# Optimization experiments

Measured on AMD Instinct MI355X. Metric: run time of the kernel, lower is better.

## Reference

```python
import jax, jax.numpy as jnp
import numpy as np

T, H, E, I = 1024, 2048, 64, 1024          # tokens, hidden, routed experts, expert ffn dim
N_GROUP, TOPK_GROUP, TOP_K = 8, 4, 8
N_SHARED = 2
ROUTED_SCALE = 2.5
IS = I * N_SHARED                            # shared-expert intermediate size


def setup_inputs() -> dict:
    key = jax.random.key(0)
    ks = jax.random.split(key, 8)
    s = 0.02
    return {
        "hidden_states": jax.random.normal(ks[0], (T, H), jnp.float32),
        "gate_w": jax.random.normal(ks[1], (E, H), jnp.float32) * s,
        "e_bias": jax.random.normal(ks[2], (E,), jnp.float32) * s,
        "w_gate": jax.random.normal(ks[3], (E, I, H), jnp.float32) * s,
        "w_up": jax.random.normal(ks[4], (E, I, H), jnp.float32) * s,
        "w_down": jax.random.normal(ks[5], (E, H, I), jnp.float32) * s,
        "shared_w_gate_up": jax.random.normal(ks[6], (2 * IS, H), jnp.float32) * s,
        "shared_w_down": jax.random.normal(ks[7], (H, IS), jnp.float32) * s,
    }


def _grouped_topk(scores, bias):
    """DeepSeek noaux_tc grouped top-k: sigmoid scores + correction bias,
    pick top `TOPK_GROUP` groups by sum of their top-2 biased scores,
    then top-K experts among allowed groups; weights from unbiased scores."""
    Tn, En = scores.shape
    s = scores + bias[None, :]                                   # [T, E]
    g = s.reshape(Tn, N_GROUP, En // N_GROUP)                    # [T, G, E/G]
    group_scores = jnp.sum(jax.lax.top_k(g, 2)[0], axis=-1)      # [T, G]
    _, gidx = jax.lax.top_k(group_scores, TOPK_GROUP)            # [T, topk_group]
    gmask = jnp.zeros((Tn, N_GROUP), scores.dtype).at[
        jnp.arange(Tn)[:, None], gidx].set(1.0)                  # [T, G]
    smask = jnp.repeat(gmask, En // N_GROUP, axis=1)             # [T, E]
    masked = jnp.where(smask > 0, s, -jnp.inf)
    _, topk_ids = jax.lax.top_k(masked, TOP_K)                   # [T, K]
    w = jnp.take_along_axis(scores, topk_ids, axis=1)            # unbiased scores
    w = w / jnp.sum(w, axis=-1, keepdims=True)                   # renormalize (norm_topk_prob)
    return w, topk_ids


def reference(hidden_states, gate_w, e_bias, w_gate, w_up, w_down,
              shared_w_gate_up, shared_w_down):
    x = hidden_states                                            # [T, H]
    router_logits = x @ gate_w.T                                 # [T, E]
    scores = jax.nn.sigmoid(router_logits)
    topk_w, topk_ids = _grouped_topk(scores, e_bias)             # [T, K] each
    # sparse combine weights [T, E] (zero for unselected experts)
    cw = jnp.zeros((x.shape[0], E), x.dtype).at[
        jnp.arange(x.shape[0])[:, None], topk_ids].add(topk_w)
    # routed experts: dense grouped-GEMM form of the fused-MoE math
    g = jnp.einsum('th,eih->tei', x, w_gate)                     # [T, E, I]
    u = jnp.einsum('th,eih->tei', x, w_up)
    h = jax.nn.silu(g) * u
    routed = jnp.einsum('tei,te,ehi->th', h, cw, w_down)         # [T, H]
    # shared experts MLP (SiluAndMul)
    sg_u = x @ shared_w_gate_up.T                                # [T, 2*IS]
    sg, su = jnp.split(sg_u, 2, axis=-1)
    shared = (jax.nn.silu(sg) * su) @ shared_w_down.T            # [T, H]
    return routed * ROUTED_SCALE + shared
```

## Files before the change

kernel.cpp:

```cpp
#include <hip/hip_runtime.h>
#include <hip/hip_bf16.h>
#include <math.h>

#define T_TOK 1024
#define HID   2048
#define NEXP  64
#define IDIM  1024
#define ISH   2048
#define TOPK  8

typedef float  f32x4  __attribute__((ext_vector_type(4)));
typedef __bf16 bf16x8 __attribute__((ext_vector_type(8)));

#define BM  128
#define BN_ 64
#define BK  64

#define BARRIER_NODRAIN() asm volatile("s_waitcnt lgkmcnt(0)\n\ts_barrier" ::: "memory")

__device__ __forceinline__ bf16x8 cvt8(f32x4 a, f32x4 b) {
  bf16x8 v;
  v[0]=(__bf16)a[0]; v[1]=(__bf16)a[1]; v[2]=(__bf16)a[2]; v[3]=(__bf16)a[3];
  v[4]=(__bf16)b[0]; v[5]=(__bf16)b[1]; v[6]=(__bf16)b[2]; v[7]=(__bf16)b[3];
  return v;
}

__global__ void init_kernel(int* counts) {
  if (threadIdx.x < NEXP) counts[threadIdx.x] = 0;
}

__global__ void xcast_kernel(const float* __restrict__ x, __bf16* __restrict__ xb) {
  long i = ((long)blockIdx.x * 256 + threadIdx.x) * 8;
  f32x4 a = *(const f32x4*)(x + i);
  f32x4 b = *(const f32x4*)(x + i + 4);
  *(bf16x8*)(xb + i) = cvt8(a, b);
}

__global__ __launch_bounds__(256)
void router_kernel(const float* __restrict__ x, const float* __restrict__ gw,
                   const float* __restrict__ eb,
                   int* __restrict__ ids, float* __restrict__ wts,
                   int* __restrict__ counts)
{
  __shared__ __align__(16) float xs[HID];
  __shared__ float red[256];
  __shared__ float sc[NEXP], sb[NEXP];
  const int t = blockIdx.x, tid = threadIdx.x;

  const f32x4* xsrc = (const f32x4*)(x + (long)t * HID);
  f32x4* xd = (f32x4*)xs;
  xd[tid]       = xsrc[tid];
  xd[tid + 256] = xsrc[tid + 256];
  __syncthreads();

  const int e = tid & 63, part = tid >> 6;
  const f32x4* wrow = (const f32x4*)(gw + (long)e * HID + part * 512);
  const f32x4* xrow = (const f32x4*)(xs + part * 512);
  float s = 0.f;
  #pragma unroll 4
  for (int j = 0; j < 128; ++j) {
    f32x4 wv = wrow[j], xv = xrow[j];
    s += wv[0]*xv[0] + wv[1]*xv[1] + wv[2]*xv[2] + wv[3]*xv[3];
  }
  red[tid] = s;
  __syncthreads();
  if (part == 0) {
    float logit = red[e] + red[e+64] + red[e+128] + red[e+192];
    float sig = 1.f / (1.f + expf(-logit));
    sc[e] = sig; sb[e] = sig + eb[e];
  }
  __syncthreads();

  if (tid == 0) {
    float gsc[8];
    for (int g = 0; g < 8; ++g) {
      float m1 = -1e30f, m2 = -1e30f;
      for (int j = 0; j < 8; ++j) {
        float v = sb[g*8 + j];
        if (v > m1) { m2 = m1; m1 = v; } else if (v > m2) m2 = v;
      }
      gsc[g] = m1 + m2;
    }
    unsigned gmask = 0;
    for (int it = 0; it < 4; ++it) {
      int best = 0; float bv = -1e30f;
      for (int g = 0; g < 8; ++g)
        if (!((gmask >> g) & 1) && gsc[g] > bv) { bv = gsc[g]; best = g; }
      gmask |= 1u << best;
    }
    unsigned long long taken = 0;
    int id8[8]; float wsum = 0.f;
    for (int it = 0; it < 8; ++it) {
      int best = 0; float bv = -1e30f;
      for (int e2 = 0; e2 < 64; ++e2) {
        if (!((gmask >> (e2 >> 3)) & 1)) continue;
        if ((taken >> e2) & 1) continue;
        float v = sb[e2];
        if (v > bv) { bv = v; best = e2; }
      }
      taken |= 1ull << best;
      id8[it] = best; wsum += sc[best];
    }
    float inv = 2.5f / wsum;
    for (int k = 0; k < 8; ++k) {
      ids[t*8 + k] = id8[k];
      wts[t*8 + k] = sc[id8[k]] * inv;
      atomicAdd(&counts[id8[k]], 1);
    }
  }
}

__global__ void scan_kernel(const int* __restrict__ counts,
                            int* __restrict__ seg_off, int* __restrict__ cursors,
                            int* __restrict__ pair_e, int* __restrict__ pair_mt,
                            int* __restrict__ npairs) {
  if (threadIdx.x == 0) {
    int off = 0, np = 0;
    for (int e = 0; e < NEXP; ++e) {
      seg_off[e] = off; cursors[e] = off;
      int c = counts[e]; off += c;
      for (int m = 0; m * BM < c; ++m) { pair_e[np] = e; pair_mt[np] = m; ++np; }
    }
    npairs[0] = np;
  }
}

__global__ void scatter_kernel(const int* __restrict__ ids, const float* __restrict__ wts,
                               int* __restrict__ cursors,
                               int* __restrict__ tok_list, float* __restrict__ wgt_list,
                               int* __restrict__ pos_of) {
  int idx = blockIdx.x * 256 + threadIdx.x;
  if (idx >= T_TOK * TOPK) return;
  int t = idx >> 3;
  int e = ids[idx];
  int pos = atomicAdd(&cursors[e], 1);
  tok_list[pos] = t;
  wgt_list[pos] = wts[idx];
  pos_of[idx] = pos;
}

template<int EPI, bool ROUTED, bool GATHER>
__global__ __launch_bounds__(256, 1)
void gemm_dma(const __bf16* __restrict__ A, const float* __restrict__ Bg0,
              const float* __restrict__ Bu0, long strideBe, int ldB, int K,
              void* Cg, void* Cu, int ldc,
              const int* __restrict__ pair_e, const int* __restrict__ pair_mt,
              const int* __restrict__ npairs,
              const int* __restrict__ seg_off, const int* __restrict__ seg_cnt,
              const int* __restrict__ tok_list, int Mfull)
{
  __shared__ __align__(16) char smem[3 * 32768];
  const int tid = threadIdx.x, lane = tid & 63, wv = tid >> 6;

  int e, mt0, soff, cnt;
  if (ROUTED) {
    int p = blockIdx.y;
    if (p >= npairs[0]) return;
    e = pair_e[p]; mt0 = pair_mt[p]; soff = seg_off[e]; cnt = seg_cnt[e];
  } else {
    e = 0; mt0 = blockIdx.y; soff = 0; cnt = Mfull;
  }
  const int rem = cnt - mt0 * BM;
  if (rem <= 0) return;

  const float* B0 = (gridDim.z == 2 && blockIdx.z) ? Bu0 : Bg0;
  void* Cout      = (gridDim.z == 2 && blockIdx.z) ? Cu  : Cg;
  const float* Bb0 = B0 + (long)e * strideBe;

  const __bf16* srcA[4];
  const float*  srcB[4];
  #pragma unroll
  for (int i = 0; i < 4; ++i) {
    int row = wv * 32 + i * 8 + (lane >> 3);
    int kcA = (lane & 7) ^ (row & 7);
    int rr  = (row < rem) ? row : (rem - 1);
    int idx = soff + mt0 * BM + rr;
    long arow = GATHER ? (long)tok_list[idx] : (long)idx;
    srcA[i] = A + arow * (long)K + kcA * 8;

    int col = wv * 16 + i * 4 + (lane >> 4);
    int kcB = (lane & 15) ^ (col & 15);
    srcB[i] = Bb0 + (long)(blockIdx.x * BN_ + col) * ldB + kcB * 4;
  }

#define STAGE(b, kk) { \
  char* Ad = smem + (b) * 32768 + wv * 4096; \
  char* Bd = Ad + 16384; \
  _Pragma("unroll") \
  for (int i = 0; i < 4; ++i) \
    __builtin_amdgcn_global_load_lds((const __attribute__((address_space(1))) void*)(srcA[i] + (kk)), \
        (__attribute__((address_space(3))) void*)(Ad + i * 1024), 16, 0, 0); \
  _Pragma("unroll") \
  for (int i = 0; i < 4; ++i) \
    __builtin_amdgcn_global_load_lds((const __attribute__((address_space(1))) void*)(srcB[i] + (kk)), \
        (__attribute__((address_space(3))) void*)(Bd + i * 1024), 16, 0, 0); }

  f32x4 acc[8] = {};
  const int c15 = lane & 15, hi = lane >> 4;

#define COMPUTE(b) { \
  char* Ab = smem + (b) * 32768; \
  char* Bbuf = Ab + 16384; \
  _Pragma("unroll") \
  for (int kh = 0; kh < 2; ++kh) { \
    const int colL = wv * 16 + c15; \
    const int kc = kh * 8 + hi * 2; \
    f32x4 b0 = *(const f32x4*)(Bbuf + colL * 256 + (((kc    ) ^ c15) << 4)); \
    f32x4 b1 = *(const f32x4*)(Bbuf + colL * 256 + (((kc + 1) ^ c15) << 4)); \
    bf16x8 bfrag = cvt8(b0, b1); \
    const int physA = ((kh * 4 + hi) ^ (lane & 7)) << 4; \
    _Pragma("unroll") \
    for (int m = 0; m < 8; ++m) { \
      bf16x8 af = *(const bf16x8*)(Ab + (m * 16 + c15) * 128 + physA); \
      acc[m] = __builtin_amdgcn_mfma_f32_16x16x32_bf16(af, bfrag, acc[m], 0, 0, 0); \
    } \
  } }

  const int NT = K / BK;
  STAGE(0, 0);
  STAGE(1, BK);
  for (int t = 0; t < NT; ++t) {
    asm volatile("s_waitcnt vmcnt(8)" ::: "memory");
    BARRIER_NODRAIN();
    const int kk = (t + 2 < NT) ? (t + 2) * BK : 0;
    STAGE((t + 2) % 3, kk);
    COMPUTE(t % 3);
  }
#undef STAGE
#undef COMPUTE

  asm volatile("s_waitcnt vmcnt(0)" ::: "memory");
  BARRIER_NODRAIN();

  if (EPI == 0) {
    __bf16* Cs = (__bf16*)smem;
    #pragma unroll
    for (int m = 0; m < 8; ++m) {
      #pragma unroll
      for (int r = 0; r < 4; ++r) {
        int row = m * 16 + hi * 4 + r;
        Cs[row * 64 + wv * 16 + c15] = (__bf16)acc[m][r];
      }
    }
    BARRIER_NODRAIN();
    __bf16* Cb = (__bf16*)Cout;
    #pragma unroll
    for (int p = 0; p < 4; ++p) {
      int row = p * 32 + (tid >> 3);
      if (row < rem)
        *(bf16x8*)(Cb + (long)(soff + mt0 * BM + row) * ldc + blockIdx.x * BN_ + (tid & 7) * 8) =
            *(const bf16x8*)&Cs[row * 64 + (tid & 7) * 8];
    }
  } else {
    float* O = (float*)Cout;
    const int col = blockIdx.x * BN_ + wv * 16 + c15;
    #pragma unroll
    for (int m = 0; m < 8; ++m) {
      #pragma unroll
      for (int r = 0; r < 4; ++r) {
        int row = m * 16 + hi * 4 + r;
        if (row < rem)
          O[(long)(mt0 * BM + row) * ldc + col] = acc[m][r];
      }
    }
  }
}

__global__ void fuse_kernel(__bf16* __restrict__ g, const __bf16* __restrict__ u,
                            const float* __restrict__ wrow, int rshift) {
  long idx = ((long)blockIdx.x * 256 + threadIdx.x) * 8;
  bf16x8 gv = *(bf16x8*)(g + idx);
  bf16x8 uv = *(const bf16x8*)(u + idx);
  float w = wrow ? wrow[idx >> rshift] : 1.f;
  bf16x8 h;
  #pragma unroll
  for (int j = 0; j < 8; ++j) {
    float gf = (float)gv[j], uf = (float)uv[j];
    h[j] = (__bf16)(w * gf * uf / (1.f + __expf(-gf)));
  }
  *(bf16x8*)(g + idx) = h;
}

__global__ __launch_bounds__(256)
void combine_kernel(const __bf16* __restrict__ y, const int* __restrict__ pos_of,
                    float* __restrict__ out) {
  const int t = blockIdx.x;
  const int c0 = threadIdx.x * 8;
  float* orow = out + (long)t * HID + c0;
  f32x4 s0 = *(const f32x4*)orow;
  f32x4 s1 = *(const f32x4*)(orow + 4);
  #pragma unroll
  for (int k = 0; k < TOPK; ++k) {
    int row = pos_of[t * TOPK + k];
    bf16x8 v = *(const bf16x8*)(y + (long)row * HID + c0);
    s0[0] += (float)v[0]; s0[1] += (float)v[1]; s0[2] += (float)v[2]; s0[3] += (float)v[3];
    s1[0] += (float)v[4]; s1[1] += (float)v[5]; s1[2] += (float)v[6]; s1[3] += (float)v[7];
  }
  *(f32x4*)orow = s0;
  *(f32x4*)(orow + 4) = s1;
}

extern "C" void kernel_launch(void* const* d_in, const int* in_sizes, int n_in,
                              void* d_out, int out_size, void* d_ws, size_t ws_size,
                              hipStream_t stream) {
  const float* x      = (const float*)d_in[0];
  const float* gate_w = (const float*)d_in[1];
  const float* e_bias = (const float*)d_in[2];
  const float* w_gate = (const float*)d_in[3];
  const float* w_up   = (const float*)d_in[4];
  const float* w_down = (const float*)d_in[5];
  const float* sw_gu  = (const float*)d_in[6];
  const float* sw_d   = (const float*)d_in[7];
  float* out = (float*)d_out;
  char* ws = (char*)d_ws;

  size_t off = 0;
  __bf16* x_bf = (__bf16*)(ws + off);        off += (size_t)T_TOK * HID * 2;
  int*    ids  = (int*)(ws + off);           off += T_TOK * TOPK * 4;
  float*  wts  = (float*)(ws + off);         off += T_TOK * TOPK * 4;
  int* counts  = (int*)(ws + off);           off += 256;
  int* segoff  = (int*)(ws + off);           off += 256;
  int* cursors = (int*)(ws + off);           off += 256;
  int* pair_e  = (int*)(ws + off);           off += 1024;
  int* pair_mt = (int*)(ws + off);           off += 1024;
  int* npairs  = (int*)(ws + off);           off += 256;
  int* tok_list = (int*)(ws + off);          off += T_TOK * TOPK * 4;
  float* wgt_list = (float*)(ws + off);      off += T_TOK * TOPK * 4;
  int* pos_of  = (int*)(ws + off);           off += T_TOK * TOPK * 4;
  off = (off + 255) & ~(size_t)255;
  __bf16* g_buf  = (__bf16*)(ws + off);      off += (size_t)T_TOK * TOPK * IDIM * 2;
  __bf16* u_buf  = (__bf16*)(ws + off);      off += (size_t)T_TOK * TOPK * IDIM * 2;
  __bf16* gs_buf = (__bf16*)(ws + off);      off += (size_t)T_TOK * ISH * 2;
  __bf16* us_buf = (__bf16*)(ws + off);      off += (size_t)T_TOK * ISH * 2;
  __bf16* y_buf  = (__bf16*)(ws + off);      off += (size_t)T_TOK * TOPK * HID * 2;

  init_kernel<<<1, 64, 0, stream>>>(counts);
  xcast_kernel<<<(T_TOK * HID) / (256 * 8), 256, 0, stream>>>(x, x_bf);
  router_kernel<<<T_TOK, 256, 0, stream>>>(x, gate_w, e_bias, ids, wts, counts);
  scan_kernel<<<1, 64, 0, stream>>>(counts, segoff, cursors, pair_e, pair_mt, npairs);
  scatter_kernel<<<(T_TOK * TOPK + 255) / 256, 256, 0, stream>>>(
      ids, wts, cursors, tok_list, wgt_list, pos_of);

  gemm_dma<0, true, true><<<dim3(IDIM / BN_, 128, 2), 256, 0, stream>>>(
      x_bf, w_gate, w_up, (long)IDIM * HID, HID, HID, g_buf, u_buf, IDIM,
      pair_e, pair_mt, npairs, segoff, counts, tok_list, 0);

  fuse_kernel<<<(T_TOK * TOPK * IDIM) / (256 * 8), 256, 0, stream>>>(g_buf, u_buf, wgt_list, 10);

  gemm_dma<0, false, false><<<dim3(ISH / BN_, T_TOK / BM, 2), 256, 0, stream>>>(
      x_bf, sw_gu, sw_gu + (size_t)ISH * HID, 0, HID, HID, gs_buf, us_buf, ISH,
      nullptr, nullptr, nullptr, nullptr, nullptr, nullptr, T_TOK);
  fuse_kernel<<<(T_TOK * ISH) / (256 * 8), 256, 0, stream>>>(gs_buf, us_buf, nullptr, 11);

  gemm_dma<2, false, false><<<dim3(HID / BN_, T_TOK / BM, 1), 256, 0, stream>>>(
      gs_buf, sw_d, sw_d, 0, ISH, ISH, out, out, HID,
      nullptr, nullptr, nullptr, nullptr, nullptr, nullptr, T_TOK);

  gemm_dma<0, true, false><<<dim3(HID / BN_, 128, 1), 256, 0, stream>>>(
      g_buf, w_down, w_down, (long)HID * IDIM, IDIM, IDIM, y_buf, y_buf, HID,
      pair_e, pair_mt, npairs, segoff, counts, tok_list, 0);

  combine_kernel<<<T_TOK, 256, 0, stream>>>(y_buf, pos_of, out);
}
```

Baseline: 653.4 us.

## Split K across waves in GEMM and reduce partial tiles through LDS

The GEMM kernel changes from splitting the output tile's N columns across waves to an intra-block split-K. Each wave now owns a 32-wide K slice of every 128-deep step and computes the full 128x64 tile using its own double-buffered LDS region. Because no wave reads another wave's staged data, the per-step block barriers go away, and each A fragment is reused across four MFMAs. The cost is four times the accumulator registers (32 f32x4 per wave), 128 KB of LDS, and a final cross-wave reduction through LDS before the store.

```diff
diff --git a/kernel.cpp b/kernel.cpp
--- a/kernel.cpp
+++ b/kernel.cpp
@@ -14,9 +14,6 @@
 
 #define BM  128
 #define BN_ 64
-#define BK  64
-
-#define BARRIER_NODRAIN() asm volatile("s_waitcnt lgkmcnt(0)\n\ts_barrier" ::: "memory")
 
 __device__ __forceinline__ bf16x8 cvt8(f32x4 a, f32x4 b) {
   bf16x8 v;
@@ -141,16 +138,17 @@
 
 template<int EPI, bool ROUTED, bool GATHER>
 __global__ __launch_bounds__(256, 1)
-void gemm_dma(const __bf16* __restrict__ A, const float* __restrict__ Bg0,
-              const float* __restrict__ Bu0, long strideBe, int ldB, int K,
-              void* Cg, void* Cu, int ldc,
-              const int* __restrict__ pair_e, const int* __restrict__ pair_mt,
-              const int* __restrict__ npairs,
-              const int* __restrict__ seg_off, const int* __restrict__ seg_cnt,
-              const int* __restrict__ tok_list, int Mfull)
+void gemm_ks(const __bf16* __restrict__ A, const float* __restrict__ Bg0,
+             const float* __restrict__ Bu0, long strideBe, int ldB, int K,
+             void* Cg, void* Cu, int ldc,
+             const int* __restrict__ pair_e, const int* __restrict__ pair_mt,
+             const int* __restrict__ npairs,
+             const int* __restrict__ seg_off, const int* __restrict__ seg_cnt,
+             const int* __restrict__ tok_list, int Mfull)
 {
-  __shared__ __align__(16) char smem[3 * 32768];
+  __shared__ __align__(16) char smem[4 * 32768];
   const int tid = threadIdx.x, lane = tid & 63, wv = tid >> 6;
+  const int c15 = lane & 15, hi = lane >> 4;
 
   int e, mt0, soff, cnt;
   if (ROUTED) {
@@ -167,100 +165,102 @@
   void* Cout      = (gridDim.z == 2 && blockIdx.z) ? Cu  : Cg;
   const float* Bb0 = B0 + (long)e * strideBe;
 
-  const __bf16* srcA[4];
-  const float*  srcB[4];
-  #pragma unroll
-  for (int i = 0; i < 4; ++i) {
-    int row = wv * 32 + i * 8 + (lane >> 3);
-    int kcA = (lane & 7) ^ (row & 7);
+  char* Wb = smem + wv * 32768;
+
+  const __bf16* srcA[8];
+  const float*  srcB[8];
+  #pragma unroll
+  for (int i = 0; i < 8; ++i) {
+    int row = i * 16 + (lane >> 2);
+    int kcA = (lane & 3) ^ (row & 3);
     int rr  = (row < rem) ? row : (rem - 1);
     int idx = soff + mt0 * BM + rr;
     long arow = GATHER ? (long)tok_list[idx] : (long)idx;
-    srcA[i] = A + arow * (long)K + kcA * 8;
-
-    int col = wv * 16 + i * 4 + (lane >> 4);
-    int kcB = (lane & 15) ^ (col & 15);
-    srcB[i] = Bb0 + (long)(blockIdx.x * BN_ + col) * ldB + kcB * 4;
+    srcA[i] = A + arow * (long)K + wv * 32 + kcA * 8;
+
+    int col = i * 8 + (lane >> 3);
+    int kcB = (lane & 7) ^ (col & 7);
+    srcB[i] = Bb0 + (long)(blockIdx.x * BN_ + col) * ldB + wv * 32 + kcB * 4;
   }
 
 #define STAGE(b, kk) { \
-  char* Ad = smem + (b) * 32768 + wv * 4096; \
-  char* Bd = Ad + 16384; \
+  char* Ad = Wb + (b) * 16384; \
+  char* Bd = Ad + 8192; \
   _Pragma("unroll") \
-  for (int i = 0; i < 4; ++i) \
+  for (int i = 0; i < 8; ++i) \
     __builtin_amdgcn_global_load_lds((const __attribute__((address_space(1))) void*)(srcA[i] + (kk)), \
         (__attribute__((address_space(3))) void*)(Ad + i * 1024), 16, 0, 0); \
   _Pragma("unroll") \
-  for (int i = 0; i < 4; ++i) \
+  for (int i = 0; i < 8; ++i) \
     __builtin_amdgcn_global_load_lds((const __attribute__((address_space(1))) void*)(srcB[i] + (kk)), \
         (__attribute__((address_space(3))) void*)(Bd + i * 1024), 16, 0, 0); }
 
-  f32x4 acc[8] = {};
-  const int c15 = lane & 15, hi = lane >> 4;
+  f32x4 acc[8][4] = {};
 
 #define COMPUTE(b) { \
-  char* Ab = smem + (b) * 32768; \
-  char* Bbuf = Ab + 16384; \
+  const char* Al = Wb + (b) * 16384; \
+  const char* Bl = Al + 8192; \
+  bf16x8 bfrag[4]; \
   _Pragma("unroll") \
-  for (int kh = 0; kh < 2; ++kh) { \
-    const int colL = wv * 16 + c15; \
-    const int kc = kh * 8 + hi * 2; \
-    f32x4 b0 = *(const f32x4*)(Bbuf + colL * 256 + (((kc    ) ^ c15) << 4)); \
-    f32x4 b1 = *(const f32x4*)(Bbuf + colL * 256 + (((kc + 1) ^ c15) << 4)); \
-    bf16x8 bfrag = cvt8(b0, b1); \
-    const int physA = ((kh * 4 + hi) ^ (lane & 7)) << 4; \
+  for (int n = 0; n < 4; ++n) { \
+    int col = n * 16 + c15; \
+    f32x4 b0 = *(const f32x4*)(Bl + col * 128 + (((hi * 2    ) ^ (col & 7)) << 4)); \
+    f32x4 b1 = *(const f32x4*)(Bl + col * 128 + (((hi * 2 + 1) ^ (col & 7)) << 4)); \
+    bfrag[n] = cvt8(b0, b1); \
+  } \
+  _Pragma("unroll") \
+  for (int m = 0; m < 8; ++m) { \
+    int row = m * 16 + c15; \
+    bf16x8 af = *(const bf16x8*)(Al + row * 64 + ((hi ^ (row & 3)) << 4)); \
     _Pragma("unroll") \
-    for (int m = 0; m < 8; ++m) { \
-      bf16x8 af = *(const bf16x8*)(Ab + (m * 16 + c15) * 128 + physA); \
-      acc[m] = __builtin_amdgcn_mfma_f32_16x16x32_bf16(af, bfrag, acc[m], 0, 0, 0); \
-    } \
+    for (int n = 0; n < 4; ++n) \
+      acc[m][n] = __builtin_amdgcn_mfma_f32_16x16x32_bf16(af, bfrag[n], acc[m][n], 0, 0, 0); \
   } }
 
-  const int NT = K / BK;
+  const int S = K / 128;
   STAGE(0, 0);
-  STAGE(1, BK);
-  for (int t = 0; t < NT; ++t) {
-    asm volatile("s_waitcnt vmcnt(8)" ::: "memory");
-    BARRIER_NODRAIN();
-    const int kk = (t + 2 < NT) ? (t + 2) * BK : 0;
-    STAGE((t + 2) % 3, kk);
-    COMPUTE(t % 3);
+  for (int s = 0; s < S; ++s) {
+    if (s + 1 < S) {
+      STAGE((s + 1) & 1, (s + 1) * 128);
+      asm volatile("s_waitcnt vmcnt(16)" ::: "memory");
+    } else {
+      asm volatile("s_waitcnt vmcnt(0)" ::: "memory");
+    }
+    COMPUTE(s & 1);
   }
 #undef STAGE
 #undef COMPUTE
 
-  asm volatile("s_waitcnt vmcnt(0)" ::: "memory");
-  BARRIER_NODRAIN();
-
-  if (EPI == 0) {
-    __bf16* Cs = (__bf16*)smem;
+  float* Pw = (float*)Wb;
+  #pragma unroll
+  for (int m = 0; m < 8; ++m)
     #pragma unroll
-    for (int m = 0; m < 8; ++m) {
+    for (int n = 0; n < 4; ++n)
       #pragma unroll
-      for (int r = 0; r < 4; ++r) {
-        int row = m * 16 + hi * 4 + r;
-        Cs[row * 64 + wv * 16 + c15] = (__bf16)acc[m][r];
-      }
-    }
-    BARRIER_NODRAIN();
-    __bf16* Cb = (__bf16*)Cout;
-    #pragma unroll
-    for (int p = 0; p < 4; ++p) {
-      int row = p * 32 + (tid >> 3);
-      if (row < rem)
-        *(bf16x8*)(Cb + (long)(soff + mt0 * BM + row) * ldc + blockIdx.x * BN_ + (tid & 7) * 8) =
-            *(const bf16x8*)&Cs[row * 64 + (tid & 7) * 8];
-    }
-  } else {
-    float* O = (float*)Cout;
-    const int col = blockIdx.x * BN_ + wv * 16 + c15;
-    #pragma unroll
-    for (int m = 0; m < 8; ++m) {
-      #pragma unroll
-      for (int r = 0; r < 4; ++r) {
-        int row = m * 16 + hi * 4 + r;
-        if (row < rem)
-          O[(long)(mt0 * BM + row) * ldc + col] = acc[m][r];
+      for (int r = 0; r < 4; ++r)
+        Pw[(m * 16 + hi * 4 + r) * 64 + n * 16 + c15] = acc[m][n][r];
+  __syncthreads();
+
+  const f32x4* P0 = (const f32x4*)(smem);
+  const f32x4* P1 = (const f32x4*)(smem + 32768);
+  const f32x4* P2 = (const f32x4*)(smem + 65536);
+  const f32x4* P3 = (const f32x4*)(smem + 98304);
+  #pragma unroll
+  for (int j = 0; j < 4; ++j) {
+    int a = j * 2048 + tid * 8;
+    int q = a >> 2;
+    f32x4 v0 = P0[q]     + P1[q]     + P2[q]     + P3[q];
+    f32x4 v1 = P0[q + 1] + P1[q + 1] + P2[q + 1] + P3[q + 1];
+    int row = a >> 6, col = a & 63;
+    if (row < rem) {
+      if (EPI == 0) {
+        __bf16* Cb = (__bf16*)Cout;
+        *(bf16x8*)(Cb + (long)(soff + mt0 * BM + row) * ldc + blockIdx.x * BN_ + col) = cvt8(v0, v1);
+      } else {
+        float* O = (float*)Cout;
+        float* dst = O + (long)(mt0 * BM + row) * ldc + blockIdx.x * BN_ + col;
+        *(f32x4*)dst = v0;
+        *(f32x4*)(dst + 4) = v1;
       }
     }
   }
@@ -341,22 +341,22 @@
   scatter_kernel<<<(T_TOK * TOPK + 255) / 256, 256, 0, stream>>>(
       ids, wts, cursors, tok_list, wgt_list, pos_of);
 
-  gemm_dma<0, true, true><<<dim3(IDIM / BN_, 128, 2), 256, 0, stream>>>(
+  gemm_ks<0, true, true><<<dim3(IDIM / BN_, 128, 2), 256, 0, stream>>>(
       x_bf, w_gate, w_up, (long)IDIM * HID, HID, HID, g_buf, u_buf, IDIM,
       pair_e, pair_mt, npairs, segoff, counts, tok_list, 0);
 
   fuse_kernel<<<(T_TOK * TOPK * IDIM) / (256 * 8), 256, 0, stream>>>(g_buf, u_buf, wgt_list, 10);
 
-  gemm_dma<0, false, false><<<dim3(ISH / BN_, T_TOK / BM, 2), 256, 0, stream>>>(
+  gemm_ks<0, false, false><<<dim3(ISH / BN_, T_TOK / BM, 2), 256, 0, stream>>>(
       x_bf, sw_gu, sw_gu + (size_t)ISH * HID, 0, HID, HID, gs_buf, us_buf, ISH,
       nullptr, nullptr, nullptr, nullptr, nullptr, nullptr, T_TOK);
   fuse_kernel<<<(T_TOK * ISH) / (256 * 8), 256, 0, stream>>>(gs_buf, us_buf, nullptr, 11);
 
-  gemm_dma<2, false, false><<<dim3(HID / BN_, T_TOK / BM, 1), 256, 0, stream>>>(
+  gemm_ks<2, false, false><<<dim3(HID / BN_, T_TOK / BM, 1), 256, 0, stream>>>(
       gs_buf, sw_d, sw_d, 0, ISH, ISH, out, out, HID,
       nullptr, nullptr, nullptr, nullptr, nullptr, nullptr, T_TOK);
 
-  gemm_dma<0, true, false><<<dim3(HID / BN_, 128, 1), 256, 0, stream>>>(
+  gemm_ks<0, true, false><<<dim3(HID / BN_, 128, 1), 256, 0, stream>>>(
       g_buf, w_down, w_down, (long)HID * IDIM, IDIM, IDIM, y_buf, y_buf, HID,
       pair_e, pair_mt, npairs, segoff, counts, tok_list, 0);
 
```

After: 651.0 us (median of 2 runs). About the same (-0.4%).

## Fuse gate/up GEMMs with SiLU epilogue, shrink BK, remap grid for L2 reuse

Applied to the files above, without the earlier changes.

Gate and up projections now run in one GEMM kernel that stages both weight tiles per K-step, accumulates into two accumulator sets, and applies the routing-weighted SiLU-and-mul in the epilogue. This removes the separate fuse kernels and the extra write and read of the g/u intermediate buffers. BK drops from 64 to 32 and launch bounds allow two blocks per CU to restore latency hiding. A 1D grid with a swizzled mapping groups eight M-tiles per N-tile, aiming to reuse weights in cache. The costs are more accumulator registers and more barriers per unit of K.

```diff
diff --git a/kernel.cpp b/kernel.cpp
--- a/kernel.cpp
+++ b/kernel.cpp
@@ -14,7 +14,7 @@
 
 #define BM  128
 #define BN_ 64
-#define BK  64
+#define BK  32
 
 #define BARRIER_NODRAIN() asm volatile("s_waitcnt lgkmcnt(0)\n\ts_barrier" ::: "memory")
 
@@ -139,88 +139,114 @@
   pos_of[idx] = pos;
 }
 
-template<int EPI, bool ROUTED, bool GATHER>
-__global__ __launch_bounds__(256, 1)
-void gemm_dma(const __bf16* __restrict__ A, const float* __restrict__ Bg0,
-              const float* __restrict__ Bu0, long strideBe, int ldB, int K,
-              void* Cg, void* Cu, int ldc,
-              const int* __restrict__ pair_e, const int* __restrict__ pair_mt,
-              const int* __restrict__ npairs,
-              const int* __restrict__ seg_off, const int* __restrict__ seg_cnt,
-              const int* __restrict__ tok_list, int Mfull)
+template<int NS, int EPI, bool ROUTED, bool GATHER>
+__global__ __launch_bounds__(256, 2)
+void gemm_x(const __bf16* __restrict__ A, const float* __restrict__ Bg0,
+            const float* __restrict__ Bu0, long strideBe, int ldB, int K,
+            void* __restrict__ Cout, int ldc, int NTB,
+            const int* __restrict__ pair_e, const int* __restrict__ pair_mt,
+            const int* __restrict__ npairs,
+            const int* __restrict__ seg_off, const int* __restrict__ seg_cnt,
+            const int* __restrict__ tok_list, const float* __restrict__ wgt_list,
+            int Mfull)
 {
-  __shared__ __align__(16) char smem[3 * 32768];
+  constexpr int BUFSZ = (1 + NS) * 8192;
+  __shared__ __align__(16) char smem[3 * BUFSZ];
+  __shared__ float sWs[BM];
   const int tid = threadIdx.x, lane = tid & 63, wv = tid >> 6;
+  const int c15 = lane & 15, hi = lane >> 4;
+
+  const int wgid = blockIdx.x;
+  const int nt   = (wgid >> 3) % NTB;
+  const int p    = (wgid / (8 * NTB)) * 8 + (wgid & 7);
 
   int e, mt0, soff, cnt;
   if (ROUTED) {
-    int p = blockIdx.y;
     if (p >= npairs[0]) return;
     e = pair_e[p]; mt0 = pair_mt[p]; soff = seg_off[e]; cnt = seg_cnt[e];
   } else {
-    e = 0; mt0 = blockIdx.y; soff = 0; cnt = Mfull;
+    if (p >= Mfull / BM) return;
+    e = 0; mt0 = p; soff = 0; cnt = Mfull;
   }
   const int rem = cnt - mt0 * BM;
   if (rem <= 0) return;
 
-  const float* B0 = (gridDim.z == 2 && blockIdx.z) ? Bu0 : Bg0;
-  void* Cout      = (gridDim.z == 2 && blockIdx.z) ? Cu  : Cg;
-  const float* Bb0 = B0 + (long)e * strideBe;
-
-  const __bf16* srcA[4];
-  const float*  srcB[4];
+  const __bf16* srcA[2];
   #pragma unroll
-  for (int i = 0; i < 4; ++i) {
-    int row = wv * 32 + i * 8 + (lane >> 3);
-    int kcA = (lane & 7) ^ (row & 7);
+  for (int i = 0; i < 2; ++i) {
+    int ia  = wv * 2 + i;
+    int row = ia * 16 + (lane >> 2);
+    int kq  = (lane & 3) ^ (row & 3);
     int rr  = (row < rem) ? row : (rem - 1);
     int idx = soff + mt0 * BM + rr;
     long arow = GATHER ? (long)tok_list[idx] : (long)idx;
-    srcA[i] = A + arow * (long)K + kcA * 8;
-
-    int col = wv * 16 + i * 4 + (lane >> 4);
-    int kcB = (lane & 15) ^ (col & 15);
-    srcB[i] = Bb0 + (long)(blockIdx.x * BN_ + col) * ldB + kcB * 4;
+    srcA[i] = A + arow * (long)K + kq * 8;
+  }
+  const float* srcB0[2];
+  const float* srcB1[2];
+  {
+    const float* Bb0 = Bg0 + (long)e * strideBe;
+    const float* Bb1 = Bu0 + (long)e * strideBe;
+    #pragma unroll
+    for (int i = 0; i < 2; ++i) {
+      int ib  = wv * 2 + i;
+      int col = ib * 8 + (lane >> 3);
+      int kq  = (lane & 7) ^ (col & 7);
+      long boff = (long)(nt * BN_ + col) * ldB + kq * 4;
+      srcB0[i] = Bb0 + boff;
+      srcB1[i] = Bb1 + boff;
+    }
   }
 
 #define STAGE(b, kk) { \
-  char* Ad = smem + (b) * 32768 + wv * 4096; \
-  char* Bd = Ad + 16384; \
+  char* base_ = smem + (b) * BUFSZ; \
   _Pragma("unroll") \
-  for (int i = 0; i < 4; ++i) \
+  for (int i = 0; i < 2; ++i) \
     __builtin_amdgcn_global_load_lds((const __attribute__((address_space(1))) void*)(srcA[i] + (kk)), \
-        (__attribute__((address_space(3))) void*)(Ad + i * 1024), 16, 0, 0); \
+        (__attribute__((address_space(3))) void*)(base_ + (wv * 2 + i) * 1024), 16, 0, 0); \
   _Pragma("unroll") \
-  for (int i = 0; i < 4; ++i) \
-    __builtin_amdgcn_global_load_lds((const __attribute__((address_space(1))) void*)(srcB[i] + (kk)), \
-        (__attribute__((address_space(3))) void*)(Bd + i * 1024), 16, 0, 0); }
-
-  f32x4 acc[8] = {};
-  const int c15 = lane & 15, hi = lane >> 4;
+  for (int i = 0; i < 2; ++i) \
+    __builtin_amdgcn_global_load_lds((const __attribute__((address_space(1))) void*)(srcB0[i] + (kk)), \
+        (__attribute__((address_space(3))) void*)(base_ + 8192 + (wv * 2 + i) * 1024), 16, 0, 0); \
+  if constexpr (NS == 2) { \
+    _Pragma("unroll") \
+    for (int i = 0; i < 2; ++i) \
+      __builtin_amdgcn_global_load_lds((const __attribute__((address_space(1))) void*)(srcB1[i] + (kk)), \
+          (__attribute__((address_space(3))) void*)(base_ + 16384 + (wv * 2 + i) * 1024), 16, 0, 0); \
+  } }
+
+  f32x4 accg[8] = {};
+  f32x4 accu[8] = {};
 
 #define COMPUTE(b) { \
-  char* Ab = smem + (b) * 32768; \
-  char* Bbuf = Ab + 16384; \
+  const char* base_ = smem + (b) * BUFSZ; \
+  const int cb = ((wv * 2 + (c15 >> 3)) << 10) + ((c15 & 7) << 7); \
+  const int cx = c15 & 7; \
+  const char* Bl0 = base_ + 8192; \
+  f32x4 g0 = *(const f32x4*)(Bl0 + cb + ((((hi * 2)    ) ^ cx) << 4)); \
+  f32x4 g1 = *(const f32x4*)(Bl0 + cb + ((((hi * 2) + 1) ^ cx) << 4)); \
+  bf16x8 bg = cvt8(g0, g1); \
+  bf16x8 bu = bg; \
+  if constexpr (NS == 2) { \
+    const char* Bl1 = base_ + 16384; \
+    f32x4 u0 = *(const f32x4*)(Bl1 + cb + ((((hi * 2)    ) ^ cx) << 4)); \
+    f32x4 u1 = *(const f32x4*)(Bl1 + cb + ((((hi * 2) + 1) ^ cx) << 4)); \
+    bu = cvt8(u0, u1); \
+  } \
   _Pragma("unroll") \
-  for (int kh = 0; kh < 2; ++kh) { \
-    const int colL = wv * 16 + c15; \
-    const int kc = kh * 8 + hi * 2; \
-    f32x4 b0 = *(const f32x4*)(Bbuf + colL * 256 + (((kc    ) ^ c15) << 4)); \
-    f32x4 b1 = *(const f32x4*)(Bbuf + colL * 256 + (((kc + 1) ^ c15) << 4)); \
-    bf16x8 bfrag = cvt8(b0, b1); \
-    const int physA = ((kh * 4 + hi) ^ (lane & 7)) << 4; \
-    _Pragma("unroll") \
-    for (int m = 0; m < 8; ++m) { \
-      bf16x8 af = *(const bf16x8*)(Ab + (m * 16 + c15) * 128 + physA); \
-      acc[m] = __builtin_amdgcn_mfma_f32_16x16x32_bf16(af, bfrag, acc[m], 0, 0, 0); \
-    } \
+  for (int m = 0; m < 8; ++m) { \
+    bf16x8 af = *(const bf16x8*)(base_ + (m << 10) + (((c15 << 2) + (hi ^ (c15 & 3))) << 4)); \
+    accg[m] = __builtin_amdgcn_mfma_f32_16x16x32_bf16(af, bg, accg[m], 0, 0, 0); \
+    if constexpr (NS == 2) \
+      accu[m] = __builtin_amdgcn_mfma_f32_16x16x32_bf16(af, bu, accu[m], 0, 0, 0); \
   } }
 
   const int NT = K / BK;
   STAGE(0, 0);
   STAGE(1, BK);
   for (int t = 0; t < NT; ++t) {
-    asm volatile("s_waitcnt vmcnt(8)" ::: "memory");
+    if constexpr (NS == 2) asm volatile("s_waitcnt vmcnt(6)" ::: "memory");
+    else                   asm volatile("s_waitcnt vmcnt(4)" ::: "memory");
     BARRIER_NODRAIN();
     const int kk = (t + 2 < NT) ? (t + 2) * BK : 0;
     STAGE((t + 2) % 3, kk);
@@ -229,56 +255,54 @@
 #undef STAGE
 #undef COMPUTE
 
+  if constexpr (NS == 2) {
+    if (tid < BM) {
+      int rr = (tid < rem) ? tid : (rem - 1);
+      sWs[tid] = ROUTED ? wgt_list[soff + mt0 * BM + rr] : 1.f;
+    }
+  }
   asm volatile("s_waitcnt vmcnt(0)" ::: "memory");
-  BARRIER_NODRAIN();
-
-  if (EPI == 0) {
+  __syncthreads();
+
+  if constexpr (EPI == 0) {
     __bf16* Cs = (__bf16*)smem;
     #pragma unroll
     for (int m = 0; m < 8; ++m) {
       #pragma unroll
       for (int r = 0; r < 4; ++r) {
         int row = m * 16 + hi * 4 + r;
-        Cs[row * 64 + wv * 16 + c15] = (__bf16)acc[m][r];
+        float v;
+        if constexpr (NS == 2) {
+          float g = accg[m][r], u = accu[m][r];
+          v = sWs[row] * g * u / (1.f + __expf(-g));
+        } else {
+          v = accg[m][r];
+        }
+        Cs[row * 64 + wv * 16 + c15] = (__bf16)v;
       }
     }
-    BARRIER_NODRAIN();
+    __syncthreads();
     __bf16* Cb = (__bf16*)Cout;
     #pragma unroll
-    for (int p = 0; p < 4; ++p) {
-      int row = p * 32 + (tid >> 3);
+    for (int p2 = 0; p2 < 4; ++p2) {
+      int row = p2 * 32 + (tid >> 3);
       if (row < rem)
-        *(bf16x8*)(Cb + (long)(soff + mt0 * BM + row) * ldc + blockIdx.x * BN_ + (tid & 7) * 8) =
+        *(bf16x8*)(Cb + (long)(soff + mt0 * BM + row) * ldc + nt * BN_ + (tid & 7) * 8) =
             *(const bf16x8*)&Cs[row * 64 + (tid & 7) * 8];
     }
   } else {
     float* O = (float*)Cout;
-    const int col = blockIdx.x * BN_ + wv * 16 + c15;
+    const int col = nt * BN_ + wv * 16 + c15;
     #pragma unroll
     for (int m = 0; m < 8; ++m) {
       #pragma unroll
       for (int r = 0; r < 4; ++r) {
         int row = m * 16 + hi * 4 + r;
         if (row < rem)
-          O[(long)(mt0 * BM + row) * ldc + col] = acc[m][r];
+          O[(long)(mt0 * BM + row) * ldc + col] = accg[m][r];
       }
     }
   }
-}
-
-__global__ void fuse_kernel(__bf16* __restrict__ g, const __bf16* __restrict__ u,
-                            const float* __restrict__ wrow, int rshift) {
-  long idx = ((long)blockIdx.x * 256 + threadIdx.x) * 8;
-  bf16x8 gv = *(bf16x8*)(g + idx);
-  bf16x8 uv = *(const bf16x8*)(u + idx);
-  float w = wrow ? wrow[idx >> rshift] : 1.f;
-  bf16x8 h;
-  #pragma unroll
-  for (int j = 0; j < 8; ++j) {
-    float gf = (float)gv[j], uf = (float)uv[j];
-    h[j] = (__bf16)(w * gf * uf / (1.f + __expf(-gf)));
-  }
-  *(bf16x8*)(g + idx) = h;
 }
 
 __global__ __launch_bounds__(256)
@@ -328,10 +352,8 @@
   float* wgt_list = (float*)(ws + off);      off += T_TOK * TOPK * 4;
   int* pos_of  = (int*)(ws + off);           off += T_TOK * TOPK * 4;
   off = (off + 255) & ~(size_t)255;
-  __bf16* g_buf  = (__bf16*)(ws + off);      off += (size_t)T_TOK * TOPK * IDIM * 2;
-  __bf16* u_buf  = (__bf16*)(ws + off);      off += (size_t)T_TOK * TOPK * IDIM * 2;
-  __bf16* gs_buf = (__bf16*)(ws + off);      off += (size_t)T_TOK * ISH * 2;
-  __bf16* us_buf = (__bf16*)(ws + off);      off += (size_t)T_TOK * ISH * 2;
+  __bf16* h_buf  = (__bf16*)(ws + off);      off += (size_t)T_TOK * TOPK * IDIM * 2;
+  __bf16* hs_buf = (__bf16*)(ws + off);      off += (size_t)T_TOK * ISH * 2;
   __bf16* y_buf  = (__bf16*)(ws + off);      off += (size_t)T_TOK * TOPK * HID * 2;
 
   init_kernel<<<1, 64, 0, stream>>>(counts);
@@ -341,24 +363,21 @@
   scatter_kernel<<<(T_TOK * TOPK + 255) / 256, 256, 0, stream>>>(
       ids, wts, cursors, tok_list, wgt_list, pos_of);
 
-  gemm_dma<0, true, true><<<dim3(IDIM / BN_, 128, 2), 256, 0, stream>>>(
-      x_bf, w_gate, w_up, (long)IDIM * HID, HID, HID, g_buf, u_buf, IDIM,
-      pair_e, pair_mt, npairs, segoff, counts, tok_list, 0);
-
-  fuse_kernel<<<(T_TOK * TOPK * IDIM) / (256 * 8), 256, 0, stream>>>(g_buf, u_buf, wgt_list, 10);
-
-  gemm_dma<0, false, false><<<dim3(ISH / BN_, T_TOK / BM, 2), 256, 0, stream>>>(
-      x_bf, sw_gu, sw_gu + (size_t)ISH * HID, 0, HID, HID, gs_buf, us_buf, ISH,
-      nullptr, nullptr, nullptr, nullptr, nullptr, nullptr, T_TOK);
-  fuse_kernel<<<(T_TOK * ISH) / (256 * 8), 256, 0, stream>>>(gs_buf, us_buf, nullptr, 11);
-
-  gemm_dma<2, false, false><<<dim3(HID / BN_, T_TOK / BM, 1), 256, 0, stream>>>(
-      gs_buf, sw_d, sw_d, 0, ISH, ISH, out, out, HID,
-      nullptr, nullptr, nullptr, nullptr, nullptr, nullptr, T_TOK);
-
-  gemm_dma<0, true, false><<<dim3(HID / BN_, 128, 1), 256, 0, stream>>>(
-      g_buf, w_down, w_down, (long)HID * IDIM, IDIM, IDIM, y_buf, y_buf, HID,
-      pair_e, pair_mt, npairs, segoff, counts, tok_list, 0);
+  gemm_x<2, 0, true, true><<<128 * 16, 256, 0, stream>>>(
+      x_bf, w_gate, w_up, (long)IDIM * HID, HID, HID, h_buf, IDIM, 16,
+      pair_e, pair_mt, npairs, segoff, counts, tok_list, wgt_list, 0);
+
+  gemm_x<2, 0, false, false><<<8 * 32, 256, 0, stream>>>(
+      x_bf, sw_gu, sw_gu + (size_t)ISH * HID, 0, HID, HID, hs_buf, ISH, 32,
+      nullptr, nullptr, nullptr, nullptr, nullptr, nullptr, nullptr, T_TOK);
+
+  gemm_x<1, 2, false, false><<<8 * 32, 256, 0, stream>>>(
+      hs_buf, sw_d, sw_d, 0, ISH, ISH, out, HID, 32,
+      nullptr, nullptr, nullptr, nullptr, nullptr, nullptr, nullptr, T_TOK);
+
+  gemm_x<1, 0, true, false><<<128 * 32, 256, 0, stream>>>(
+      h_buf, w_down, w_down, (long)HID * IDIM, IDIM, IDIM, y_buf, HID, 32,
+      pair_e, pair_mt, npairs, segoff, counts, tok_list, wgt_list, 0);
 
   combine_kernel<<<T_TOK, 256, 0, stream>>>(y_buf, pos_of, out);
 }
```

After: 691.0 us. +5.8%, slower.

## Restructure MoE GEMM pipeline with decoupled A/B staging and narrower N tiles

Applied to the files above, without the earlier changes.

Replaces the 3-stage lockstep A/B load pipeline with separate rings: a deep 7-buffer ring of 32-wide K slices for A and a 3-buffer ring of wide K super-steps for B (fp32 weights). The issue of loads is spread across inner iterations so there is always outstanding DMA. The gate/up GEMMs switch to BN=32 with split M per wave to double the grid's block count. This targets memory latency stalls and low occupancy from one-block-per-CU tiles, at the cost of more complex index bookkeeping, more LDS and smaller per-wave MFMA reuse.

```diff
diff --git a/kernel.cpp b/kernel.cpp
--- a/kernel.cpp
+++ b/kernel.cpp
@@ -13,8 +13,6 @@
 typedef __bf16 bf16x8 __attribute__((ext_vector_type(8)));
 
 #define BM  128
-#define BN_ 64
-#define BK  64
 
 #define BARRIER_NODRAIN() asm volatile("s_waitcnt lgkmcnt(0)\n\ts_barrier" ::: "memory")
 
@@ -139,18 +137,32 @@
   pos_of[idx] = pos;
 }
 
-template<int EPI, bool ROUTED, bool GATHER>
+template<int BN, int SK, int EPI, bool ROUTED, bool GATHER>
 __global__ __launch_bounds__(256, 1)
-void gemm_dma(const __bf16* __restrict__ A, const float* __restrict__ Bg0,
-              const float* __restrict__ Bu0, long strideBe, int ldB, int K,
-              void* Cg, void* Cu, int ldc,
-              const int* __restrict__ pair_e, const int* __restrict__ pair_mt,
-              const int* __restrict__ npairs,
-              const int* __restrict__ seg_off, const int* __restrict__ seg_cnt,
-              const int* __restrict__ tok_list, int Mfull)
+void gemm_ps(const __bf16* __restrict__ A, const float* __restrict__ Bg0,
+             const float* __restrict__ Bu0, long strideBe, int ldB, int K,
+             void* Cg, void* Cu, int ldc,
+             const int* __restrict__ pair_e, const int* __restrict__ pair_mt,
+             const int* __restrict__ npairs,
+             const int* __restrict__ seg_off, const int* __restrict__ seg_cnt,
+             const int* __restrict__ tok_list, int Mfull)
 {
-  __shared__ __align__(16) char smem[3 * 32768];
+  constexpr int INNER = SK / 32;
+  constexpr int NBI   = 8 / INNER;
+  constexpr int MR    = (BN == 32) ? 4 : 8;
+  constexpr int AH    = (BN == 32) ? 5 : 4;
+  constexpr int CNT   = AH * (NBI + 2);
+  constexpr int RPI   = (BN == 32) ? 1 : 2;
+  constexpr int CH    = 1024 / RPI;
+  constexpr int CM    = CH / 16 - 1;
+
+  __shared__ __align__(16) char sB[3][BN * CH];
+  __shared__ __align__(16) char sA[7][8192];
+
   const int tid = threadIdx.x, lane = tid & 63, wv = tid >> 6;
+  const int c15 = lane & 15, hi = lane >> 4;
+  const int colg = (BN == 32) ? (wv >> 1) * 16 : wv * 16;
+  const int row0 = (BN == 32) ? (wv & 1) * 64 : 0;
 
   int e, mt0, soff, cnt;
   if (ROUTED) {
@@ -165,100 +177,110 @@
 
   const float* B0 = (gridDim.z == 2 && blockIdx.z) ? Bu0 : Bg0;
   void* Cout      = (gridDim.z == 2 && blockIdx.z) ? Cu  : Cg;
-  const float* Bb0 = B0 + (long)e * strideBe;
-
-  const __bf16* srcA[4];
-  const float*  srcB[4];
-  #pragma unroll
-  for (int i = 0; i < 4; ++i) {
-    int row = wv * 32 + i * 8 + (lane >> 3);
-    int kcA = (lane & 7) ^ (row & 7);
+  const float* Bb = B0 + (long)e * strideBe + (long)(blockIdx.x * BN) * ldB;
+
+  const __bf16* srcA[2];
+  #pragma unroll
+  for (int i = 0; i < 2; ++i) {
+    int row = (wv * 2 + i) * 16 + (lane >> 2);
+    int kc  = (lane & 3) ^ (row & 3);
     int rr  = (row < rem) ? row : (rem - 1);
     int idx = soff + mt0 * BM + rr;
     long arow = GATHER ? (long)tok_list[idx] : (long)idx;
-    srcA[i] = A + arow * (long)K + kcA * 8;
-
-    int col = wv * 16 + i * 4 + (lane >> 4);
-    int kcB = (lane & 15) ^ (col & 15);
-    srcB[i] = Bb0 + (long)(blockIdx.x * BN_ + col) * ldB + kcB * 4;
-  }
-
-#define STAGE(b, kk) { \
-  char* Ad = smem + (b) * 32768 + wv * 4096; \
-  char* Bd = Ad + 16384; \
+    srcA[i] = A + arow * (long)K + kc * 8;
+  }
+
+#define ISSUE_B(q, bd, ssk) { \
+  int r0_ = (BN == 32) ? (wv * 8 + (q)) : (wv * 16 + (q) * 2); \
+  int row_ = r0_ + ((RPI == 2) ? (lane >> 5) : 0); \
+  int chunk_ = ((RPI == 2) ? (lane & 31) : lane) ^ (row_ & CM); \
+  const float* src_ = Bb + (long)row_ * ldB + (ssk) + chunk_ * 4; \
+  __builtin_amdgcn_global_load_lds((const __attribute__((address_space(1))) void*)src_, \
+      (__attribute__((address_space(3))) void*)(&sB[bd][r0_ * CH]), 16, 0, 0); }
+
+#define ISSUE_A(ta, NTt_) { \
+  int ad_ = (ta) % 7; \
+  int ka_ = (((ta) < (NTt_)) ? (ta) : ((NTt_) - 1)) * 32; \
   _Pragma("unroll") \
-  for (int i = 0; i < 4; ++i) \
-    __builtin_amdgcn_global_load_lds((const __attribute__((address_space(1))) void*)(srcA[i] + (kk)), \
-        (__attribute__((address_space(3))) void*)(Ad + i * 1024), 16, 0, 0); \
+  for (int i = 0; i < 2; ++i) \
+    __builtin_amdgcn_global_load_lds((const __attribute__((address_space(1))) void*)(srcA[i] + ka_), \
+        (__attribute__((address_space(3))) void*)(&sA[ad_][(wv * 2 + i) * 1024]), 16, 0, 0); }
+
+  f32x4 acc[MR] = {};
+
+#define COMPUTE(ab, bb, tl) { \
+  const char* Bl_ = sB[bb]; \
+  const int col_ = colg + c15; \
+  const int c0_ = (tl) * 8 + hi * 2; \
+  f32x4 b0_ = *(const f32x4*)(Bl_ + col_ * CH + (((c0_    ) ^ (col_ & CM)) << 4)); \
+  f32x4 b1_ = *(const f32x4*)(Bl_ + col_ * CH + (((c0_ + 1) ^ (col_ & CM)) << 4)); \
+  bf16x8 bf_ = cvt8(b0_, b1_); \
+  const char* Al_ = sA[ab]; \
   _Pragma("unroll") \
-  for (int i = 0; i < 4; ++i) \
-    __builtin_amdgcn_global_load_lds((const __attribute__((address_space(1))) void*)(srcB[i] + (kk)), \
-        (__attribute__((address_space(3))) void*)(Bd + i * 1024), 16, 0, 0); }
-
-  f32x4 acc[8] = {};
-  const int c15 = lane & 15, hi = lane >> 4;
-
-#define COMPUTE(b) { \
-  char* Ab = smem + (b) * 32768; \
-  char* Bbuf = Ab + 16384; \
-  _Pragma("unroll") \
-  for (int kh = 0; kh < 2; ++kh) { \
-    const int colL = wv * 16 + c15; \
-    const int kc = kh * 8 + hi * 2; \
-    f32x4 b0 = *(const f32x4*)(Bbuf + colL * 256 + (((kc    ) ^ c15) << 4)); \
-    f32x4 b1 = *(const f32x4*)(Bbuf + colL * 256 + (((kc + 1) ^ c15) << 4)); \
-    bf16x8 bfrag = cvt8(b0, b1); \
-    const int physA = ((kh * 4 + hi) ^ (lane & 7)) << 4; \
-    _Pragma("unroll") \
-    for (int m = 0; m < 8; ++m) { \
-      bf16x8 af = *(const bf16x8*)(Ab + (m * 16 + c15) * 128 + physA); \
-      acc[m] = __builtin_amdgcn_mfma_f32_16x16x32_bf16(af, bfrag, acc[m], 0, 0, 0); \
-    } \
+  for (int m = 0; m < MR; ++m) { \
+    int row_ = row0 + m * 16 + c15; \
+    bf16x8 af_ = *(const bf16x8*)(Al_ + row_ * 64 + ((hi ^ (row_ & 3)) << 4)); \
+    acc[m] = __builtin_amdgcn_mfma_f32_16x16x32_bf16(af_, bf_, acc[m], 0, 0, 0); \
   } }
 
-  const int NT = K / BK;
-  STAGE(0, 0);
-  STAGE(1, BK);
-  for (int t = 0; t < NT; ++t) {
-    asm volatile("s_waitcnt vmcnt(8)" ::: "memory");
+  const int NSS = K / SK;
+  const int NTt = NSS * INNER;
+
+  #pragma unroll
+  for (int q = 0; q < 8; ++q) ISSUE_B(q, 0, 0);
+  for (int j = 0; j < AH; ++j) ISSUE_A(j, NTt);
+  #pragma unroll
+  for (int q = 0; q < 8; ++q) ISSUE_B(q, 1, SK);
+
+  for (int t = 0; t < NTt; ++t) {
+    int pB  = (t > 0) ? (t - 1) : 0;
+    int pss = pB / INNER + 2;
+    int bd  = pss % 3;
+    int ssk = (((pss < NSS) ? pss : (NSS - 1))) * SK;
+    int qb  = (pB % INNER) * NBI;
+    ISSUE_B(qb, bd, ssk);
+    if (NBI == 2) ISSUE_B(qb + 1, bd, ssk);
+    ISSUE_A(t + AH, NTt);
+    asm volatile("s_waitcnt vmcnt(%0)" :: "i"(CNT) : "memory");
     BARRIER_NODRAIN();
-    const int kk = (t + 2 < NT) ? (t + 2) * BK : 0;
-    STAGE((t + 2) % 3, kk);
-    COMPUTE(t % 3);
-  }
-#undef STAGE
+    COMPUTE(t % 7, (t / INNER) % 3, t % INNER);
+  }
+#undef ISSUE_B
+#undef ISSUE_A
 #undef COMPUTE
 
   asm volatile("s_waitcnt vmcnt(0)" ::: "memory");
-  BARRIER_NODRAIN();
-
-  if (EPI == 0) {
-    __bf16* Cs = (__bf16*)smem;
+  __syncthreads();
+
+  if constexpr (EPI == 0) {
+    __bf16* Cs = (__bf16*)&sB[0][0];
     #pragma unroll
-    for (int m = 0; m < 8; ++m) {
+    for (int m = 0; m < MR; ++m) {
       #pragma unroll
       for (int r = 0; r < 4; ++r) {
-        int row = m * 16 + hi * 4 + r;
-        Cs[row * 64 + wv * 16 + c15] = (__bf16)acc[m][r];
-      }
-    }
-    BARRIER_NODRAIN();
+        int row = row0 + m * 16 + hi * 4 + r;
+        Cs[row * BN + colg + c15] = (__bf16)acc[m][r];
+      }
+    }
+    __syncthreads();
     __bf16* Cb = (__bf16*)Cout;
-    #pragma unroll
-    for (int p = 0; p < 4; ++p) {
-      int row = p * 32 + (tid >> 3);
-      if (row < rem)
-        *(bf16x8*)(Cb + (long)(soff + mt0 * BM + row) * ldc + blockIdx.x * BN_ + (tid & 7) * 8) =
-            *(const bf16x8*)&Cs[row * 64 + (tid & 7) * 8];
+    const int row = tid >> 1, half = tid & 1;
+    if (row < rem) {
+      __bf16* dst = Cb + (long)(soff + mt0 * BM + row) * ldc + blockIdx.x * BN;
+      #pragma unroll
+      for (int j = 0; j < BN / 16; ++j) {
+        int c8 = half * (BN / 16) + j;
+        *(bf16x8*)(dst + c8 * 8) = *(const bf16x8*)&Cs[row * BN + c8 * 8];
+      }
     }
   } else {
     float* O = (float*)Cout;
-    const int col = blockIdx.x * BN_ + wv * 16 + c15;
+    const int col = blockIdx.x * BN + colg + c15;
     #pragma unroll
-    for (int m = 0; m < 8; ++m) {
+    for (int m = 0; m < MR; ++m) {
       #pragma unroll
       for (int r = 0; r < 4; ++r) {
-        int row = m * 16 + hi * 4 + r;
+        int row = row0 + m * 16 + hi * 4 + r;
         if (row < rem)
           O[(long)(mt0 * BM + row) * ldc + col] = acc[m][r];
       }
@@ -341,22 +363,22 @@
   scatter_kernel<<<(T_TOK * TOPK + 255) / 256, 256, 0, stream>>>(
       ids, wts, cursors, tok_list, wgt_list, pos_of);
 
-  gemm_dma<0, true, true><<<dim3(IDIM / BN_, 128, 2), 256, 0, stream>>>(
+  gemm_ps<32, 256, 0, true, true><<<dim3(IDIM / 32, 128, 2), 256, 0, stream>>>(
       x_bf, w_gate, w_up, (long)IDIM * HID, HID, HID, g_buf, u_buf, IDIM,
       pair_e, pair_mt, npairs, segoff, counts, tok_list, 0);
 
   fuse_kernel<<<(T_TOK * TOPK * IDIM) / (256 * 8), 256, 0, stream>>>(g_buf, u_buf, wgt_list, 10);
 
-  gemm_dma<0, false, false><<<dim3(ISH / BN_, T_TOK / BM, 2), 256, 0, stream>>>(
+  gemm_ps<32, 256, 0, false, false><<<dim3(ISH / 32, T_TOK / BM, 2), 256, 0, stream>>>(
       x_bf, sw_gu, sw_gu + (size_t)ISH * HID, 0, HID, HID, gs_buf, us_buf, ISH,
       nullptr, nullptr, nullptr, nullptr, nullptr, nullptr, T_TOK);
   fuse_kernel<<<(T_TOK * ISH) / (256 * 8), 256, 0, stream>>>(gs_buf, us_buf, nullptr, 11);
 
-  gemm_dma<2, false, false><<<dim3(HID / BN_, T_TOK / BM, 1), 256, 0, stream>>>(
+  gemm_ps<64, 128, 2, false, false><<<dim3(HID / 64, T_TOK / BM, 1), 256, 0, stream>>>(
       gs_buf, sw_d, sw_d, 0, ISH, ISH, out, out, HID,
       nullptr, nullptr, nullptr, nullptr, nullptr, nullptr, T_TOK);
 
-  gemm_dma<0, true, false><<<dim3(HID / BN_, 128, 1), 256, 0, stream>>>(
+  gemm_ps<64, 128, 0, true, false><<<dim3(HID / 64, 128, 1), 256, 0, stream>>>(
       g_buf, w_down, w_down, (long)HID * IDIM, IDIM, IDIM, y_buf, y_buf, HID,
       pair_e, pair_mt, npairs, segoff, counts, tok_list, 0);
 
```

Measured after the change: 1.547 ms. 137% more time.
